# Optimization experiments

Measured on AMD Instinct MI355X. Metric: run time of the kernel, lower is better.

## Reference

```python
import jax, jax.numpy as jnp
import numpy as np
import math

B = 50        # graphs per batch
NPG = 2000    # nodes per graph
EPG = 12000   # edges per graph
F_IN = 256
NHID = 128
RATIO = 0.8


def setup_inputs() -> dict:
    key = jax.random.key(0)
    ks = jax.random.split(key, 12)
    N = B * NPG
    src_loc = jax.random.randint(ks[0], (B, EPG), 0, NPG)
    dst_loc = jax.random.randint(ks[1], (B, EPG), 0, NPG)
    off = (jnp.arange(B) * NPG)[:, None]
    edge_index = jnp.stack([(src_loc + off).reshape(-1), (dst_loc + off).reshape(-1)]).astype(jnp.int32)

    def lin(k, fi, fo):
        return (jax.random.normal(k, (fi, fo), jnp.float32) / np.sqrt(fi).astype(np.float32))

    return {
        "x": jax.random.normal(ks[2], (N, F_IN), jnp.float32),
        "W1": lin(ks[3], F_IN, NHID), "b1": jnp.zeros(NHID, jnp.float32),
        "Ws1": lin(ks[4], NHID, 1), "bs1": jnp.zeros(1, jnp.float32),
        "W2": lin(ks[5], NHID, NHID), "b2": jnp.zeros(NHID, jnp.float32),
        "Ws2": lin(ks[6], NHID, 1), "bs2": jnp.zeros(1, jnp.float32),
        "W3": lin(ks[7], NHID, NHID), "b3": jnp.zeros(NHID, jnp.float32),
        "Ws3": lin(ks[8], NHID, 1), "bs3": jnp.zeros(1, jnp.float32),
        "Wl": lin(ks[9], 2 * NHID, NHID), "bl": jnp.zeros(NHID, jnp.float32),
        "edge_index": edge_index,
    }


def gcn_conv(x, W, b, src, dst, w, N):
    # PyG GCNConv: D^{-1/2} (A + I) D^{-1/2} X W + b, deg from edge weights + self loop
    h = x @ W
    deg = jax.ops.segment_sum(w, dst, num_segments=N) + 1.0
    dis = jax.lax.rsqrt(deg)
    norm = w * dis[src] * dis[dst]                       # [E]
    agg = jax.ops.segment_sum(h[src] * norm[:, None], dst, num_segments=N)
    return agg + h / deg[:, None] + b                    # self-loop norm = 1/deg


def sag_pool(x, src, dst, w, Ws, bs, n_per_graph):
    N = x.shape[0]
    k = math.ceil(RATIO * n_per_graph)
    score = gcn_conv(x, Ws, bs, src, dst, w, N)[:, 0]    # [N]
    _, topi = jax.lax.top_k(score.reshape(B, n_per_graph), k)
    perm = (topi + (jnp.arange(B) * n_per_graph)[:, None]).reshape(-1)
    x_new = x[perm] * jnp.tanh(score[perm])[:, None]
    # filter_adj: keep edges whose endpoints survive, reindex; dropped edges -> weight 0
    mapping = jnp.full((N,), -1, jnp.int32).at[perm].set(jnp.arange(B * k, dtype=jnp.int32))
    ns, nd = mapping[src], mapping[dst]
    valid = (ns >= 0) & (nd >= 0) & (w > 0)
    return (x_new, jnp.where(valid, ns, 0), jnp.where(valid, nd, 0),
            jnp.where(valid, w, jnp.zeros((), x.dtype)), k)


def readout(x, n):
    # global max pool || global mean pool (equal-size graphs, nodes grouped per graph)
    xr = x.reshape(B, n, -1)
    return jnp.concatenate([xr.max(axis=1), xr.mean(axis=1)], axis=-1)


def reference(x, W1, b1, Ws1, bs1, W2, b2, Ws2, bs2, W3, b3, Ws3, bs3, Wl, bl, edge_index):
    src, dst = edge_index[0], edge_index[1]
    w = jnp.ones(src.shape[0], x.dtype)
    n = NPG
    x = jax.nn.relu(gcn_conv(x, W1, b1, src, dst, w, B * n))
    x, src, dst, w, n = sag_pool(x, src, dst, w, Ws1, bs1, n)
    x1 = readout(x, n)
    x = jax.nn.relu(gcn_conv(x, W2, b2, src, dst, w, B * n))
    x, src, dst, w, n = sag_pool(x, src, dst, w, Ws2, bs2, n)
    x2 = readout(x, n)
    x = jax.nn.relu(gcn_conv(x, W3, b3, src, dst, w, B * n))
    x, src, dst, w, n = sag_pool(x, src, dst, w, Ws3, bs3, n)
    x3 = readout(x, n)
    return jax.nn.relu((x1 + x2 + x3) @ Wl + bl)
```

## Files before the change

kernel.cpp:

```cpp
#include <hip/hip_runtime.h>
#include <math.h>

#define B_GRAPHS 50
#define NPG0     2000
#define EPG      12000
#define F_IN_C   256
#define NHID     128
#define N0       (B_GRAPHS * NPG0)
#define NE       (B_GRAPHS * EPG)
#define RSEG     32
#define GSLOTS   7
#define CPAD     136

typedef _Float16 f16x8 __attribute__((ext_vector_type(8)));
typedef float    f32x4 __attribute__((ext_vector_type(4)));

static inline int cdiv(int a, int b) { return (a + b - 1) / b; }

__global__ void k_fill_start(int* __restrict__ cnt, float* __restrict__ accum) {
    int i = blockIdx.x * 256 + threadIdx.x;
    if (i < N0) cnt[i] = 0;
    if (i < B_GRAPHS * 256) accum[i] = 0.f;
}

__global__ void k_init_cvt(const int* __restrict__ ei, int* __restrict__ esrc,
                           int* __restrict__ edst, float* __restrict__ ew,
                           int* __restrict__ cnt,
                           const float* __restrict__ W1, const float* __restrict__ W2,
                           const float* __restrict__ W3, _Float16* __restrict__ WT1,
                           _Float16* __restrict__ WT2, _Float16* __restrict__ WT3) {
    int t = blockIdx.x * 256 + threadIdx.x;
    if (t < NE) {
        int d = ei[NE + t];
        esrc[t] = ei[t]; edst[t] = d; ew[t] = 1.0f;
        atomicAdd(&cnt[d], 1);
    }
    if (t < 128 * 256) {
        int n = t >> 8, kk = t & 255;
        WT1[t] = (_Float16)W1[kk * 128 + n];
    } else if (t < 128 * 256 + 128 * 128) {
        int u = t - 32768; int n = u >> 7, kk = u & 127;
        WT2[u] = (_Float16)W2[kk * 128 + n];
    } else if (t < 128 * 256 + 2 * 128 * 128) {
        int u = t - 49152; int n = u >> 7, kk = u & 127;
        WT3[u] = (_Float16)W3[kk * 128 + n];
    }
}

template<int FP32IN, int F, int GATHER>
__global__ __launch_bounds__(256) void k_gemm_ws(const void* __restrict__ Xin,
                                                 const _Float16* __restrict__ WT,
                                                 const int* __restrict__ perm,
                                                 const float* __restrict__ gate,
                                                 _Float16* __restrict__ H, int N) {
    constexpr int KH  = (F > 128) ? 128 : F;
    constexpr int K8H = KH / 8;
    constexpr int SMEMSZ = (128 * KH > 64 * CPAD) ? 128 * KH : 64 * CPAD;
    __shared__ _Float16 smem[SMEMSZ];
    const int tid  = threadIdx.x;
    const int wave = tid >> 6, lane = tid & 63;
    const int quad = lane >> 4, l16 = lane & 15;
    const int m_blk = blockIdx.x * 64;

    f32x4 acc[8];
#pragma unroll
    for (int j = 0; j < 8; ++j) acc[j] = {0.f, 0.f, 0.f, 0.f};

    int row0 = m_blk + wave * 16 + l16;
    if (row0 > N - 1) row0 = N - 1;
    _Float16 g0 = (_Float16)1.0f;
    if (GATHER) {
        g0 = (_Float16)gate[row0];
        row0 = perm[row0];
    }
    const int sx = l16 & 7;
    constexpr int NKQ = F / 32;

    if (FP32IN) {
        constexpr int PD = (NKQ < 4) ? NKQ : 4;
        const float* base0 = (const float*)Xin + (size_t)row0 * F + quad * 8;
        float4 p0[PD][2];
#pragma unroll
        for (int i = 0; i < PD; ++i) {
            p0[i][0] = ((const float4*)(base0 + i * 32))[0];
            p0[i][1] = ((const float4*)(base0 + i * 32))[1];
        }
#pragma unroll
        for (int c = tid; c < 128 * K8H; c += 256) {
            int n = c / K8H, k8 = c - n * K8H;
            f16x8 v = *(const f16x8*)&WT[(size_t)(n * (F / 8) + k8) * 8];
            *(f16x8*)&smem[n * KH + ((k8 ^ (n & 7)) << 3)] = v;
        }
        __syncthreads();
#pragma unroll
        for (int kq = 0; kq < NKQ; ++kq) {
            if (KH < F && kq == NKQ / 2) {
                __syncthreads();
#pragma unroll
                for (int c = tid; c < 128 * K8H; c += 256) {
                    int n = c / K8H, k8 = c - n * K8H;
                    f16x8 v = *(const f16x8*)&WT[(size_t)(n * (F / 8) + K8H + k8) * 8];
                    *(f16x8*)&smem[n * KH + ((k8 ^ (n & 7)) << 3)] = v;
                }
                __syncthreads();
            }
            const int b = kq % PD;
            float4 f0 = p0[b][0], f1 = p0[b][1];
            if (kq + PD < NKQ) {
                p0[b][0] = ((const float4*)(base0 + (kq + PD) * 32))[0];
                p0[b][1] = ((const float4*)(base0 + (kq + PD) * 32))[1];
            }
            f16x8 af0 = (f16x8){(_Float16)f0.x,(_Float16)f0.y,(_Float16)f0.z,(_Float16)f0.w,
                                (_Float16)f1.x,(_Float16)f1.y,(_Float16)f1.z,(_Float16)f1.w};
            f16x8 bf[8];
#pragma unroll
            for (int j = 0; j < 8; ++j)
                bf[j] = *(const f16x8*)&smem[(j * 16 + l16) * KH + (((((kq & 3) << 2) + quad) ^ sx) << 3)];
#pragma unroll
            for (int j = 0; j < 8; ++j)
                acc[j] = __builtin_amdgcn_mfma_f32_16x16x32_f16(af0, bf[j], acc[j], 0, 0, 0);
        }
    } else {
#pragma unroll
        for (int c = tid; c < 128 * K8H; c += 256) {
            int n = c / K8H, k8 = c - n * K8H;
            f16x8 v = *(const f16x8*)&WT[(size_t)(n * K8H + k8) * 8];
            *(f16x8*)&smem[n * KH + ((k8 ^ (n & 7)) << 3)] = v;
        }
        const _Float16* base0 = (const _Float16*)Xin + (size_t)row0 * F + quad * 8;
        f16x8 q0[NKQ];
#pragma unroll
        for (int i = 0; i < NKQ; ++i)
            q0[i] = *(const f16x8*)(base0 + i * 32);
        __syncthreads();
#pragma unroll
        for (int kq = 0; kq < NKQ; ++kq) {
            f16x8 af0 = q0[kq];
            if (GATHER) af0 = af0 * g0;
            f16x8 bf[8];
#pragma unroll
            for (int j = 0; j < 8; ++j)
                bf[j] = *(const f16x8*)&smem[(j * 16 + l16) * KH + (((((kq & 3) << 2) + quad) ^ sx) << 3)];
#pragma unroll
            for (int j = 0; j < 8; ++j)
                acc[j] = __builtin_amdgcn_mfma_f32_16x16x32_f16(af0, bf[j], acc[j], 0, 0, 0);
        }
    }
    __syncthreads();

    _Float16* sC = smem;
    const int rw = wave * 16;
#pragma unroll
    for (int j = 0; j < 8; ++j)
#pragma unroll
        for (int g = 0; g < 4; ++g)
            sC[(rw + quad * 4 + g) * CPAD + j * 16 + l16] = (_Float16)acc[j][g];
    __syncthreads();
    {
        int rr = tid >> 2;
        int cc = (tid & 3) * 32;
        int gr = m_blk + rr;
        if (gr < N) {
            _Float16* Hr = H + (size_t)gr * 128 + cc;
            const _Float16* Sr = sC + rr * CPAD + cc;
#pragma unroll
            for (int c = 0; c < 4; ++c)
                *(f16x8*)&Hr[c * 8] = *(const f16x8*)&Sr[c * 8];
        }
    }
}

__global__ __launch_bounds__(256) void k_scan(const int* __restrict__ cnt,
                                              int* __restrict__ offs,
                                              int* __restrict__ cursor, int npg) {
    __shared__ int ch[256];
    int b = blockIdx.x, tid = threadIdx.x;
    int per = (npg + 255) >> 8;
    int base = b * npg;
    int s0 = tid * per;
    int s1 = s0 + per; if (s1 > npg) s1 = npg; if (s0 > npg) s0 = npg;
    int s = 0;
    for (int i = s0; i < s1; ++i) s += cnt[base + i];
    ch[tid] = s;
    __syncthreads();
    for (int d = 1; d < 256; d <<= 1) {
        int t = ch[tid] + ((tid >= d) ? ch[tid - d] : 0);
        __syncthreads();
        ch[tid] = t;
        __syncthreads();
    }
    int run = b * EPG + ch[tid] - s;
    for (int i = s0; i < s1; ++i) {
        offs[base + i] = run; cursor[base + i] = run;
        run += cnt[base + i];
    }
}

__global__ void k_fill_csr(const int* __restrict__ esrc, const int* __restrict__ edst,
                           const float* __restrict__ ew, const int* __restrict__ cnt,
                           int* __restrict__ cursor, int* __restrict__ csr_src,
                           float* __restrict__ csr_norm) {
    int e = blockIdx.x * 256 + threadIdx.x;
    if (e < NE) {
        if (ew[e] > 0.f) {
            int sN = esrc[e], d = edst[e];
            int pos = atomicAdd(&cursor[d], 1);
            csr_src[pos] = sN;
            csr_norm[pos] = rsqrtf((float)(cnt[sN] + 1)) * rsqrtf((float)(cnt[d] + 1));
        }
    }
}

__global__ __launch_bounds__(256) void k_agg(const _Float16* __restrict__ H,
                                             const int* __restrict__ csr_src,
                                             const float* __restrict__ csr_norm,
                                             const int* __restrict__ offs,
                                             const int* __restrict__ cnt,
                                             const float* __restrict__ bias,
                                             const float* __restrict__ Ws,
                                             _Float16* __restrict__ X,
                                             float* __restrict__ hs,
                                             int bpg, int npg) {
    int bi = blockIdx.x;
    int x = bi & 7, s = bi >> 3;
    int gslot = s / bpg, blk = s - gslot * bpg;
    int g = x + 8 * gslot;
    if (g >= B_GRAPHS) return;
    int node = g * npg + blk * 4 + (threadIdx.x >> 6);
    int lane = threadIdx.x & 63;
    int quad = lane >> 4, l16 = lane & 15;

    int st = offs[node], c = cnt[node], en = st + c;
    float acc[8];
#pragma unroll
    for (int j = 0; j < 8; ++j) acc[j] = 0.f;

    if (c > 0) {
        for (int e0 = st; e0 < en; e0 += 8) {
            int eA = e0 + quad, eB = eA + 4;
            int ecA = eA < en ? eA : en - 1;
            int ecB = eB < en ? eB : en - 1;
            int uA = csr_src[ecA], uB = csr_src[ecB];
            float nA = (eA < en) ? csr_norm[ecA] : 0.f;
            float nB = (eB < en) ? csr_norm[ecB] : 0.f;
            f16x8 hA = *(const f16x8*)&H[(size_t)uA * NHID + l16 * 8];
            f16x8 hB = *(const f16x8*)&H[(size_t)uB * NHID + l16 * 8];
#pragma unroll
            for (int j = 0; j < 8; ++j) acc[j] = fmaf((float)hA[j], nA, acc[j]);
#pragma unroll
            for (int j = 0; j < 8; ++j) acc[j] = fmaf((float)hB[j], nB, acc[j]);
        }
    }
#pragma unroll
    for (int j = 0; j < 8; ++j) {
        acc[j] += __shfl_xor(acc[j], 16, 64);
        acc[j] += __shfl_xor(acc[j], 32, 64);
    }
    float invd = 1.f / (float)(c + 1);
    f16x8 hn = *(const f16x8*)&H[(size_t)node * NHID + l16 * 8];
    float4 b0 = *(const float4*)&bias[l16 * 8];
    float4 b1 = *(const float4*)&bias[l16 * 8 + 4];
    float4 w0 = *(const float4*)&Ws[l16 * 8];
    float4 w1 = *(const float4*)&Ws[l16 * 8 + 4];
    const float bb[8] = {b0.x, b0.y, b0.z, b0.w, b1.x, b1.y, b1.z, b1.w};
    const float ww[8] = {w0.x, w0.y, w0.z, w0.w, w1.x, w1.y, w1.z, w1.w};
    float sd = 0.f;
    f16x8 o;
#pragma unroll
    for (int j = 0; j < 8; ++j) {
        float v = fmaxf(acc[j] + (float)hn[j] * invd + bb[j], 0.f);
        o[j] = (_Float16)v;
        sd = fmaf(v, ww[j], sd);
    }
    if (quad == 0)
        *(f16x8*)&X[(size_t)node * NHID + l16 * 8] = o;
    sd += __shfl_xor(sd, 1, 64);
    sd += __shfl_xor(sd, 2, 64);
    sd += __shfl_xor(sd, 4, 64);
    sd += __shfl_xor(sd, 8, 64);
    if (lane == 0) hs[node] = sd;
}

__global__ void k_score(const float* __restrict__ hs, const int* __restrict__ csr_src,
                        const float* __restrict__ csr_norm, const int* __restrict__ offs,
                        const int* __restrict__ cnt, const float* __restrict__ bs,
                        float* __restrict__ score, int N) {
    int i = blockIdx.x * 256 + threadIdx.x;
    if (i >= N) return;
    int s = offs[i], c = cnt[i];
    float a = 0.f;
    for (int e = s; e < s + c; ++e) a = fmaf(hs[csr_src[e]], csr_norm[e], a);
    score[i] = a + hs[i] / (float)(c + 1) + bs[0];
}

__global__ __launch_bounds__(1024) void k_topk(const float* __restrict__ score,
                                               int* __restrict__ mapping,
                                               int* __restrict__ perm,
                                               float* __restrict__ gate,
                                               int* __restrict__ cntN,
                                               int npg, int k) {
    __shared__ float ss[2048];
    __shared__ int   si[2048];
    int b = blockIdx.x, tid = threadIdx.x;
    for (int i = tid; i < 2048; i += 1024) {
        if (i < npg) { ss[i] = score[b * npg + i]; si[i] = i; }
        else         { ss[i] = -__builtin_inff();  si[i] = i; }
    }
    __syncthreads();
    for (int size = 2; size <= 2048; size <<= 1) {
        for (int stride = size >> 1; stride > 0; stride >>= 1) {
            int t = tid;
            int i = ((t & ~(stride - 1)) << 1) | (t & (stride - 1));
            int j = i | stride;
            float sa = ss[i], sb = ss[j];
            int   ia = si[i], ib = si[j];
            bool b_before_a = (sb > sa) || (sb == sa && ib < ia);
            bool forward = ((i & size) == 0);
            bool doswap = forward ? b_before_a : !b_before_a;
            if (doswap) { ss[i] = sb; ss[j] = sa; si[i] = ib; si[j] = ia; }
            __syncthreads();
        }
    }
    for (int j = tid; j < npg; j += 1024) {
        int oldg = b * npg + si[j];
        if (j < k) {
            int newg = b * k + j;
            perm[newg] = oldg;
            mapping[oldg] = newg;
            gate[newg] = tanhf(ss[j]);
        } else {
            mapping[oldg] = -1;
        }
    }
    for (int j = tid; j < k; j += 1024) cntN[b * k + j] = 0;
}

__global__ __launch_bounds__(128) void k_pool_readout(const _Float16* __restrict__ X,
                                                      const float* __restrict__ gate,
                                                      const int* __restrict__ perm,
                                                      float* __restrict__ pmax,
                                                      float* __restrict__ psum, int k) {
    int s = blockIdx.x, b = blockIdx.y, f = threadIdx.x;
    int j0 = (k * s) / RSEG, j1 = (k * (s + 1)) / RSEG;
    float mx = -__builtin_inff(), sm = 0.f;
    for (int j = j0; j < j1; ++j) {
        int g = b * k + j;
        int old = perm[g];
        float v = (float)X[(size_t)old * NHID + f] * gate[g];
        mx = fmaxf(mx, v);
        sm += v;
    }
    pmax[(size_t)(b * RSEG + s) * NHID + f] = mx;
    psum[(size_t)(b * RSEG + s) * NHID + f] = sm;
}

__global__ __launch_bounds__(128) void k_readout_comb(const float* __restrict__ pmax,
                                                      const float* __restrict__ psum,
                                                      float* __restrict__ accum, int k) {
    int b = blockIdx.x, f = threadIdx.x;
    float mx = -__builtin_inff(), sm = 0.f;
#pragma unroll
    for (int s = 0; s < RSEG; ++s) {
        mx = fmaxf(mx, pmax[(size_t)(b * RSEG + s) * NHID + f]);
        sm += psum[(size_t)(b * RSEG + s) * NHID + f];
    }
    accum[b * 256 + f]       += mx;
    accum[b * 256 + 128 + f] += sm / (float)k;
}

__global__ void k_remap(int* __restrict__ esrc, int* __restrict__ edst,
                        float* __restrict__ ew, const int* __restrict__ mapping,
                        int* __restrict__ cntN) {
    int e = blockIdx.x * 256 + threadIdx.x;
    if (e >= NE) return;
    int sN = esrc[e], d = edst[e];
    float we = ew[e];
    int ns = mapping[sN], nd = mapping[d];
    bool valid = (ns >= 0) && (nd >= 0) && (we > 0.f);
    esrc[e] = valid ? ns : 0;
    edst[e] = valid ? nd : 0;
    ew[e] = valid ? we : 0.f;
    if (valid) atomicAdd(&cntN[nd], 1);
}

__global__ __launch_bounds__(128) void k_comb_final(const float* __restrict__ pmax,
                                                    const float* __restrict__ psum,
                                                    const float* __restrict__ accum,
                                                    const float* __restrict__ Wl,
                                                    const float* __restrict__ bl,
                                                    float* __restrict__ out, int k) {
    __shared__ float a[256];
    int b = blockIdx.x, f = threadIdx.x;
    float mx = -__builtin_inff(), sm = 0.f;
#pragma unroll
    for (int s = 0; s < RSEG; ++s) {
        mx = fmaxf(mx, pmax[(size_t)(b * RSEG + s) * NHID + f]);
        sm += psum[(size_t)(b * RSEG + s) * NHID + f];
    }
    a[f]       = accum[b * 256 + f] + mx;
    a[128 + f] = accum[b * 256 + 128 + f] + sm / (float)k;
    __syncthreads();
    float s = bl[f];
    for (int i = 0; i < 256; ++i) s = fmaf(a[i], Wl[i * NHID + f], s);
    out[b * NHID + f] = fmaxf(s, 0.f);
}

extern "C" void kernel_launch(void* const* d_in, const int* in_sizes, int n_in,
                              void* d_out, int out_size, void* d_ws, size_t ws_size,
                              hipStream_t stream) {
    const float* x0 = (const float*)d_in[0];
    const float* Wm[3] = {(const float*)d_in[1], (const float*)d_in[5], (const float*)d_in[9]};
    const float* bm[3] = {(const float*)d_in[2], (const float*)d_in[6], (const float*)d_in[10]};
    const float* Wsc[3] = {(const float*)d_in[3], (const float*)d_in[7], (const float*)d_in[11]};
    const float* bsc[3] = {(const float*)d_in[4], (const float*)d_in[8], (const float*)d_in[12]};
    const float* Wl = (const float*)d_in[13];
    const float* bl = (const float*)d_in[14];
    const int*   ei = (const int*)d_in[15];
    float* out = (float*)d_out;

    _Float16* bufA = (_Float16*)d_ws;
    _Float16* bufB = bufA + (size_t)N0 * NHID;
    _Float16* WT1  = bufB + (size_t)N0 * NHID;
    _Float16* WT2  = WT1 + 128 * 256;
    _Float16* WT3  = WT2 + 128 * 128;
    float* hs     = (float*)(WT3 + 128 * 128);
    float* score  = hs + N0;
    float* gate   = score + N0;
    float* accum  = gate + N0;
    float* pmax   = accum + B_GRAPHS * 256;
    float* psum   = pmax + B_GRAPHS * RSEG * NHID;
    int*   cntA   = (int*)(psum + B_GRAPHS * RSEG * NHID);
    int*   cntB   = cntA + N0;
    int*   offs   = cntB + N0;
    int*   cursor = offs + N0;
    int*   mapping= cursor + N0;
    int*   perm   = mapping + N0;
    int*   esrc   = perm + N0;
    int*   edst   = esrc + NE;
    float* ew     = (float*)(edst + NE);
    int*   csr_src= (int*)(ew + NE);
    float* csr_norm = (float*)(csr_src + NE);

    _Float16* WTs[3] = {WT1, WT2, WT3};
    const int EG = cdiv(NE, 256);

    k_fill_start<<<cdiv(N0, 256), 256, 0, stream>>>(cntA, accum);
    k_init_cvt<<<EG, 256, 0, stream>>>(ei, esrc, edst, ew, cntA,
                                       Wm[0], Wm[1], Wm[2], WT1, WT2, WT3);

    int npg = NPG0;
    _Float16* Hbuf = bufA; _Float16* Xbuf = bufB;

    for (int layer = 0; layer < 3; ++layer) {
        int N = B_GRAPHS * npg;
        int k = (npg * 4) / 5;
        int NG = cdiv(N, 256);
        int bpg = npg >> 2;
        int* cnt  = (layer == 1) ? cntB : cntA;
        int* cntN = (layer == 1) ? cntA : cntB;

        if (layer == 0)
            k_gemm_ws<1, 256, 0><<<cdiv(N, 64), 256, 0, stream>>>(x0, WTs[0], perm, gate, Hbuf, N);
        else
            k_gemm_ws<0, 128, 1><<<cdiv(N, 64), 256, 0, stream>>>(Xbuf, WTs[layer], perm, gate, Hbuf, N);
        k_scan<<<B_GRAPHS, 256, 0, stream>>>(cnt, offs, cursor, npg);
        k_fill_csr<<<EG, 256, 0, stream>>>(esrc, edst, ew, cnt, cursor, csr_src, csr_norm);
        k_agg<<<8 * GSLOTS * bpg, 256, 0, stream>>>(Hbuf, csr_src, csr_norm, offs, cnt,
                                                    bm[layer], Wsc[layer], Xbuf, hs, bpg, npg);
        k_score<<<NG, 256, 0, stream>>>(hs, csr_src, csr_norm, offs, cnt, bsc[layer], score, N);
        k_topk<<<B_GRAPHS, 1024, 0, stream>>>(score, mapping, perm, gate, cntN, npg, k);
        k_pool_readout<<<dim3(RSEG, B_GRAPHS), 128, 0, stream>>>(Xbuf, gate, perm, pmax, psum, k);
        if (layer < 2) {
            k_remap<<<EG, 256, 0, stream>>>(esrc, edst, ew, mapping, cntN);
            k_readout_comb<<<B_GRAPHS, 128, 0, stream>>>(pmax, psum, accum, k);
        } else {
            k_comb_final<<<B_GRAPHS, 128, 0, stream>>>(pmax, psum, accum, Wl, bl, out, k);
        }

        npg = k;
    }
}
```

Baseline: 600.6 us.

## Fuse CSR scan/fill and edge remap into per-graph kernels using shared memory

Merges the per-graph prefix scan and CSR fill into one 1024-thread block per graph, with counts and cursors held in shared memory and LDS atomics replacing global ones. It also folds the edge remap and next-layer degree histogram into the top-k kernel through a shared-memory mapping, which removes the global mapping and cursor arrays and two kernel launches per layer. The cost is that edge processing now runs on only 50 blocks, one per graph, instead of a grid spread over the whole device, so parallelism drops and the top-k kernel uses more shared memory.

```diff
diff --git a/kernel.cpp b/kernel.cpp
--- a/kernel.cpp
+++ b/kernel.cpp
@@ -11,6 +11,7 @@
 #define RSEG     32
 #define GSLOTS   7
 #define CPAD     136
+#define KMAX     1600
 
 typedef _Float16 f16x8 __attribute__((ext_vector_type(8)));
 typedef float    f32x4 __attribute__((ext_vector_type(4)));
@@ -170,20 +171,27 @@
     }
 }
 
-__global__ __launch_bounds__(256) void k_scan(const int* __restrict__ cnt,
-                                              int* __restrict__ offs,
-                                              int* __restrict__ cursor, int npg) {
-    __shared__ int ch[256];
+__global__ __launch_bounds__(1024) void k_scancsr(const int* __restrict__ cnt,
+                                                  int* __restrict__ offs,
+                                                  const int* __restrict__ esrc,
+                                                  const int* __restrict__ edst,
+                                                  const float* __restrict__ ew,
+                                                  int* __restrict__ csr_src,
+                                                  float* __restrict__ csr_norm,
+                                                  int npg) {
+    __shared__ int ch[1024];
+    __shared__ int scnt[2048];
+    __shared__ int scur[2048];
     int b = blockIdx.x, tid = threadIdx.x;
-    int per = (npg + 255) >> 8;
     int base = b * npg;
+    int per = (npg + 1023) >> 10;
     int s0 = tid * per;
     int s1 = s0 + per; if (s1 > npg) s1 = npg; if (s0 > npg) s0 = npg;
     int s = 0;
-    for (int i = s0; i < s1; ++i) s += cnt[base + i];
+    for (int i = s0; i < s1; ++i) { int c = cnt[base + i]; scnt[i] = c; s += c; }
     ch[tid] = s;
     __syncthreads();
-    for (int d = 1; d < 256; d <<= 1) {
+    for (int d = 1; d < 1024; d <<= 1) {
         int t = ch[tid] + ((tid >= d) ? ch[tid - d] : 0);
         __syncthreads();
         ch[tid] = t;
@@ -191,22 +199,19 @@
     }
     int run = b * EPG + ch[tid] - s;
     for (int i = s0; i < s1; ++i) {
-        offs[base + i] = run; cursor[base + i] = run;
-        run += cnt[base + i];
-    }
-}
-
-__global__ void k_fill_csr(const int* __restrict__ esrc, const int* __restrict__ edst,
-                           const float* __restrict__ ew, const int* __restrict__ cnt,
-                           int* __restrict__ cursor, int* __restrict__ csr_src,
-                           float* __restrict__ csr_norm) {
-    int e = blockIdx.x * 256 + threadIdx.x;
-    if (e < NE) {
-        if (ew[e] > 0.f) {
-            int sN = esrc[e], d = edst[e];
-            int pos = atomicAdd(&cursor[d], 1);
+        offs[base + i] = run; scur[i] = run;
+        run += scnt[i];
+    }
+    __syncthreads();
+    int e0 = b * EPG;
+    for (int e = tid; e < EPG; e += 1024) {
+        float w = ew[e0 + e];
+        if (w > 0.f) {
+            int sN = esrc[e0 + e], d = edst[e0 + e];
+            int pos = atomicAdd(&scur[d - base], 1);
             csr_src[pos] = sN;
-            csr_norm[pos] = rsqrtf((float)(cnt[sN] + 1)) * rsqrtf((float)(cnt[d] + 1));
+            csr_norm[pos] = rsqrtf((float)(scnt[sN - base] + 1)) *
+                            rsqrtf((float)(scnt[d - base] + 1));
         }
     }
 }
@@ -293,14 +298,19 @@
     score[i] = a + hs[i] / (float)(c + 1) + bs[0];
 }
 
+template<int REMAP>
 __global__ __launch_bounds__(1024) void k_topk(const float* __restrict__ score,
-                                               int* __restrict__ mapping,
                                                int* __restrict__ perm,
                                                float* __restrict__ gate,
+                                               int* __restrict__ esrc,
+                                               int* __restrict__ edst,
+                                               float* __restrict__ ew,
                                                int* __restrict__ cntN,
                                                int npg, int k) {
     __shared__ float ss[2048];
     __shared__ int   si[2048];
+    __shared__ int   smap[2048];
+    __shared__ int   shist[KMAX];
     int b = blockIdx.x, tid = threadIdx.x;
     for (int i = tid; i < 2048; i += 1024) {
         if (i < npg) { ss[i] = score[b * npg + i]; si[i] = i; }
@@ -322,17 +332,38 @@
         }
     }
     for (int j = tid; j < npg; j += 1024) {
-        int oldg = b * npg + si[j];
+        int ol = si[j];
         if (j < k) {
             int newg = b * k + j;
-            perm[newg] = oldg;
-            mapping[oldg] = newg;
+            perm[newg] = b * npg + ol;
+            smap[ol] = newg;
             gate[newg] = tanhf(ss[j]);
         } else {
-            mapping[oldg] = -1;
-        }
-    }
-    for (int j = tid; j < k; j += 1024) cntN[b * k + j] = 0;
+            smap[ol] = -1;
+        }
+    }
+    if (REMAP) {
+        for (int j = tid; j < k; j += 1024) shist[j] = 0;
+        __syncthreads();
+        int base = b * npg, e0 = b * EPG;
+        for (int e = tid; e < EPG; e += 1024) {
+            int idx = e0 + e;
+            float w = ew[idx];
+            bool valid = false;
+            int ns = 0, nd = 0;
+            if (w > 0.f) {
+                ns = smap[esrc[idx] - base];
+                nd = smap[edst[idx] - base];
+                valid = (ns >= 0) && (nd >= 0);
+            }
+            esrc[idx] = valid ? ns : 0;
+            edst[idx] = valid ? nd : 0;
+            ew[idx]   = valid ? w : 0.f;
+            if (valid) atomicAdd(&shist[nd - b * k], 1);
+        }
+        __syncthreads();
+        for (int j = tid; j < k; j += 1024) cntN[b * k + j] = shist[j];
+    }
 }
 
 __global__ __launch_bounds__(128) void k_pool_readout(const _Float16* __restrict__ X,
@@ -368,21 +399,6 @@
     accum[b * 256 + 128 + f] += sm / (float)k;
 }
 
-__global__ void k_remap(int* __restrict__ esrc, int* __restrict__ edst,
-                        float* __restrict__ ew, const int* __restrict__ mapping,
-                        int* __restrict__ cntN) {
-    int e = blockIdx.x * 256 + threadIdx.x;
-    if (e >= NE) return;
-    int sN = esrc[e], d = edst[e];
-    float we = ew[e];
-    int ns = mapping[sN], nd = mapping[d];
-    bool valid = (ns >= 0) && (nd >= 0) && (we > 0.f);
-    esrc[e] = valid ? ns : 0;
-    edst[e] = valid ? nd : 0;
-    ew[e] = valid ? we : 0.f;
-    if (valid) atomicAdd(&cntN[nd], 1);
-}
-
 __global__ __launch_bounds__(128) void k_comb_final(const float* __restrict__ pmax,
                                                     const float* __restrict__ psum,
                                                     const float* __restrict__ accum,
@@ -432,9 +448,7 @@
     int*   cntA   = (int*)(psum + B_GRAPHS * RSEG * NHID);
     int*   cntB   = cntA + N0;
     int*   offs   = cntB + N0;
-    int*   cursor = offs + N0;
-    int*   mapping= cursor + N0;
-    int*   perm   = mapping + N0;
+    int*   perm   = offs + N0;
     int*   esrc   = perm + N0;
     int*   edst   = esrc + NE;
     float* ew     = (float*)(edst + NE);
@@ -463,15 +477,19 @@
             k_gemm_ws<1, 256, 0><<<cdiv(N, 64), 256, 0, stream>>>(x0, WTs[0], perm, gate, Hbuf, N);
         else
             k_gemm_ws<0, 128, 1><<<cdiv(N, 64), 256, 0, stream>>>(Xbuf, WTs[layer], perm, gate, Hbuf, N);
-        k_scan<<<B_GRAPHS, 256, 0, stream>>>(cnt, offs, cursor, npg);
-        k_fill_csr<<<EG, 256, 0, stream>>>(esrc, edst, ew, cnt, cursor, csr_src, csr_norm);
+        k_scancsr<<<B_GRAPHS, 1024, 0, stream>>>(cnt, offs, esrc, edst, ew,
+                                                 csr_src, csr_norm, npg);
         k_agg<<<8 * GSLOTS * bpg, 256, 0, stream>>>(Hbuf, csr_src, csr_norm, offs, cnt,
                                                     bm[layer], Wsc[layer], Xbuf, hs, bpg, npg);
         k_score<<<NG, 256, 0, stream>>>(hs, csr_src, csr_norm, offs, cnt, bsc[layer], score, N);
-        k_topk<<<B_GRAPHS, 1024, 0, stream>>>(score, mapping, perm, gate, cntN, npg, k);
+        if (layer < 2)
+            k_topk<1><<<B_GRAPHS, 1024, 0, stream>>>(score, perm, gate, esrc, edst, ew,
+                                                     cntN, npg, k);
+        else
+            k_topk<0><<<B_GRAPHS, 1024, 0, stream>>>(score, perm, gate, esrc, edst, ew,
+                                                     cntN, npg, k);
         k_pool_readout<<<dim3(RSEG, B_GRAPHS), 128, 0, stream>>>(Xbuf, gate, perm, pmax, psum, k);
         if (layer < 2) {
-            k_remap<<<EG, 256, 0, stream>>>(esrc, edst, ew, mapping, cntN);
             k_readout_comb<<<B_GRAPHS, 128, 0, stream>>>(pmax, psum, accum, k);
         } else {
             k_comb_final<<<B_GRAPHS, 128, 0, stream>>>(pmax, psum, accum, Wl, bl, out, k);
```

Result: faster. 569.2 us (-5.2%).
